# Optimization experiments

Hardware: AMD Instinct MI355X
Metric: run time of the kernel (lower is better)

The kernel has to match this reference:

```python
import jax, jax.numpy as jnp
import numpy as np

FEATURES = 256
HIDDEN = 256
NUM_BINS = 10
NUM_BLOCKS = 2
MULT = 2 * NUM_BINS + 1  # tails=None -> widths(K) + heights(K+1)
MIN_BW = 1e-3
MIN_BH = 1e-3
BATCH = 8192


def _build_masks():
    # nflows MADE sequential degrees
    in_deg = np.arange(1, FEATURES + 1)
    hid_deg = np.arange(HIDDEN) % max(1, FEATURES - 1) + min(1, FEATURES - 1)
    m0 = (hid_deg[:, None] >= in_deg[None, :]).astype(np.float32)   # [H, F]
    mh = (hid_deg[:, None] >= hid_deg[None, :]).astype(np.float32)  # [H, H]
    out_deg = np.repeat(in_deg, MULT)                               # feature-major tiling (nflows _tile)
    mf = (out_deg[:, None] > hid_deg[None, :]).astype(np.float32)   # [F*MULT, H]
    return jnp.asarray(m0), jnp.asarray(mh), jnp.asarray(mf)

MASK0, MASKH, MASKF = _build_masks()


def setup_inputs() -> dict:
    key = jax.random.key(0)
    ks = jax.random.split(key, 7)
    s = 1.0 / np.sqrt(HIDDEN)
    return {
        "inputs": jax.random.uniform(ks[0], (BATCH, FEATURES), dtype=jnp.float32),
        "W0": jax.random.normal(ks[1], (HIDDEN, FEATURES), dtype=jnp.float32) * s,
        "b0": jax.random.normal(ks[2], (HIDDEN,), dtype=jnp.float32) * 0.01,
        "Wb": jax.random.normal(ks[3], (2 * NUM_BLOCKS, HIDDEN, HIDDEN), dtype=jnp.float32) * s,
        "bb": jax.random.normal(ks[4], (2 * NUM_BLOCKS, HIDDEN), dtype=jnp.float32) * 0.01,
        "Wf": jax.random.normal(ks[5], (FEATURES * MULT, HIDDEN), dtype=jnp.float32) * s,
        "bf": jax.random.normal(ks[6], (FEATURES * MULT,), dtype=jnp.float32) * 0.01,
    }


def _made(x, W0, b0, Wb, bb, Wf, bf):
    h = x @ (W0 * MASK0).T + b0
    for i in range(NUM_BLOCKS):  # pre-activation masked residual blocks
        t = jax.nn.relu(h)
        t = t @ (Wb[2 * i] * MASKH).T + bb[2 * i]
        t = jax.nn.relu(t)
        t = t @ (Wb[2 * i + 1] * MASKH).T + bb[2 * i + 1]
        h = h + t
    return h @ (Wf * MASKF).T + bf  # [B, F*MULT]


def _quadratic_spline(x, uw, uh):
    # x: [B,F]; uw: [B,F,K]; uh: [B,F,K+1]
    widths = jax.nn.softmax(uw, axis=-1)
    widths = MIN_BW + (1.0 - MIN_BW * NUM_BINS) * widths
    hexp = jnp.exp(uh)
    area = jnp.sum(0.5 * (hexp[..., :-1] + hexp[..., 1:]) * widths, axis=-1, keepdims=True)
    heights = hexp / area
    heights = MIN_BH + (1.0 - MIN_BH) * heights

    cdf = jnp.cumsum(0.5 * (heights[..., :-1] + heights[..., 1:]) * widths, axis=-1)
    cdf = cdf.at[..., -1].set(1.0)
    cdf = jnp.pad(cdf, [(0, 0), (0, 0), (1, 0)])
    locs = jnp.cumsum(widths, axis=-1)
    locs = locs.at[..., -1].set(1.0)
    locs = jnp.pad(locs, [(0, 0), (0, 0), (1, 0)])

    # searchsorted: sum(x >= knots) - 1, clamped into valid bins
    idx = jnp.clip(jnp.sum(x[..., None] >= locs, axis=-1) - 1, 0, NUM_BINS - 1)
    g = lambda t, i: jnp.take_along_axis(t, i[..., None], axis=-1)[..., 0]

    loc = g(locs, idx)
    w = g(widths, idx)
    lcdf = g(cdf, idx)
    hl = g(heights, idx)
    hr = g(heights, idx + 1)

    a = 0.5 * (hr - hl) * w
    b = hl * w
    alpha = (x - loc) / w
    out = jnp.clip(a * alpha * alpha + b * alpha + lcdf, 0.0, 1.0)
    logabsdet = jnp.log(alpha * (hr - hl) + hl)
    return out, jnp.sum(logabsdet, axis=-1)  # sum_except_batch


def reference(inputs, W0, b0, Wb, bb, Wf, bf):
    params = _made(inputs, W0, b0, Wb, bb, Wf, bf)
    tp = params.reshape(inputs.shape[0], FEATURES, MULT)
    scale = 1.0 / np.sqrt(HIDDEN).astype(np.float32)
    uw = tp[..., :NUM_BINS] * scale
    uh = tp[..., NUM_BINS:] * scale
    return _quadratic_spline(inputs, uw, uh)
```

## Files before the change

kernel.cpp:

```cpp
#include <hip/hip_runtime.h>

typedef _Float16 f16;
typedef f16 f16x8 __attribute__((ext_vector_type(8)));
typedef float f32x4 __attribute__((ext_vector_type(4)));

#define MFMA(A,B,C) __builtin_amdgcn_mfma_f32_16x16x32_f16(A,B,C,0,0,0)

#define PTRUNK 0u
#define PHEAD  655360u

__device__ __forceinline__ void fsplit(float v, f16& hi, f16& lo) {
    hi = (f16)v;
    lo = (f16)(v - (float)hi);
}

__global__ __launch_bounds__(256) void prep_kernel(
    const float* __restrict__ W0, const float* __restrict__ Wb,
    const float* __restrict__ Wf, unsigned char* __restrict__ wsb)
{
    __shared__ f16 sm[16][264];
    const int b = blockIdx.x, t = threadIdx.x;
    const int cr = t >> 4, kc = t & 15;

    if (b < 80) {
        const int mat = b >> 4, ct = b & 15;
        const int c = ct * 16 + cr;
        const int cd = c % 255;
        const float* src = ((mat == 0) ? W0 : (Wb + (mat - 1) * 65536)) + c * 256;
        #pragma unroll
        for (int u = 0; u < 4; ++u) {
            const int k = kc * 16 + u * 4;
            float4 v = *(const float4*)(src + k);
            float vv[4] = {v.x, v.y, v.z, v.w};
            #pragma unroll
            for (int e = 0; e < 4; ++e) {
                int kk = k + e;
                int kd = (mat == 0) ? kk : (kk % 255);
                sm[cr][kk] = (cd >= kd) ? (f16)vv[e] : (f16)0.f;
            }
        }
        __syncthreads();
        const int ks = t >> 5, ln = t & 31;
        #pragma unroll
        for (int rep = 0; rep < 2; ++rep) {
            const int L = ln + rep * 32;
            const int li = L & 15, lg = L >> 4;
            f16x8 v = *(const f16x8*)&sm[li][ks * 32 + lg * 8];
            ((f16x8*)(wsb + PTRUNK))[(mat * 128 + ks * 16 + ct) * 64 + L] = v;
        }
    } else {
        const int hb = b - 80;
        const int bly = hb / 21, ct = hb - bly * 21;
        const int cl = ct * 16 + cr;
        const int fw = cl / 21;
        const int f  = bly * 16 + fw;
        const int m  = cl - fw * 21;
        const float* src = Wf + (f * 21 + m) * 256;
        #pragma unroll
        for (int u = 0; u < 4; ++u) {
            const int k = kc * 16 + u * 4;
            float4 v = *(const float4*)(src + k);
            float vv[4] = {v.x, v.y, v.z, v.w};
            #pragma unroll
            for (int e = 0; e < 4; ++e) {
                int kk = k + e;
                int jd = kk % 255;
                sm[cr][(kk + 1) & 255] = (f > jd) ? (f16)vv[e] : (f16)0.f;
            }
        }
        __syncthreads();
        const int ks = t >> 5, ln = t & 31;
        #pragma unroll
        for (int rep = 0; rep < 2; ++rep) {
            const int L = ln + rep * 32;
            const int li = L & 15, lg = L >> 4;
            f16x8 v = *(const f16x8*)&sm[li][ks * 32 + lg * 8];
            ((f16x8*)(wsb + PHEAD))[((bly * 8 + ks) * 21 + ct) * 64 + L] = v;
        }
    }
}

__global__ __launch_bounds__(256, 2) void mega_kernel(
    const float* __restrict__ x, const unsigned char* __restrict__ wsb,
    const float* __restrict__ b0, const float* __restrict__ bb,
    const float* __restrict__ bfp, float* __restrict__ out,
    float* __restrict__ lad)
{
    __shared__ f16  Ah[2][16][280];
    __shared__ f16  Al[2][16][280];
    __shared__ float prm[4][16][100];
    __shared__ float ladp[4][16];

    const int t = threadIdx.x, lane = t & 63;
    const int wu = __builtin_amdgcn_readfirstlane(t >> 6);
    const int li = lane & 15, lg = lane >> 4;
    const int r0 = blockIdx.x * 16;

    {
        int row = t >> 4, cb = (t & 15) * 16;
        const float* xr = x + (r0 + row) * 256 + cb;
        f16 hi[16], lo[16];
        #pragma unroll
        for (int j = 0; j < 16; j += 4) {
            float4 v4 = *(const float4*)(xr + j);
            fsplit(v4.x, hi[j],     lo[j]);
            fsplit(v4.y, hi[j + 1], lo[j + 1]);
            fsplit(v4.z, hi[j + 2], lo[j + 2]);
            fsplit(v4.w, hi[j + 3], lo[j + 3]);
        }
        *(f16x8*)&Ah[0][row][cb]     = *(f16x8*)&hi[0];
        *(f16x8*)&Ah[0][row][cb + 8] = *(f16x8*)&hi[8];
        *(f16x8*)&Al[0][row][cb]     = *(f16x8*)&lo[0];
        *(f16x8*)&Al[0][row][cb + 8] = *(f16x8*)&lo[8];
    }
    __syncthreads();

    const f16x8* wt = (const f16x8*)(wsb + PTRUNK);
    const f16x8* wh = (const f16x8*)(wsb + PHEAD);

    f32x4 h[4], acc[4];
    const int nkp = 2 * wu + 2;

    auto gemm = [&](int mat, int src, int add7, const float* __restrict__ bias) {
        #pragma unroll
        for (int ci = 0; ci < 4; ++ci) acc[ci] = (f32x4){0.f, 0.f, 0.f, 0.f};
        const int tot = nkp + add7;
        const f16x8* wb = wt + mat * 8192;
        f16x8 bA[4], bB[4];
        #pragma unroll
        for (int ci = 0; ci < 4; ++ci) bA[ci] = wb[(wu * 4 + ci) * 64 + lane];
        for (int s = 0; s < tot; s += 2) {
            const int ks1 = (s + 1 < nkp) ? (s + 1) : 7;
            #pragma unroll
            for (int ci = 0; ci < 4; ++ci)
                bB[ci] = wb[(ks1 * 16 + wu * 4 + ci) * 64 + lane];
            {
                const int ks = (s < nkp) ? s : 7;
                f16x8 ah = *(const f16x8*)&Ah[src][li][ks * 32 + lg * 8];
                f16x8 al = *(const f16x8*)&Al[src][li][ks * 32 + lg * 8];
                #pragma unroll
                for (int ci = 0; ci < 4; ++ci) {
                    acc[ci] = MFMA(al, bA[ci], acc[ci]);
                    acc[ci] = MFMA(ah, bA[ci], acc[ci]);
                }
            }
            const int ks2 = (s + 2 < nkp) ? (s + 2) : 7;
            #pragma unroll
            for (int ci = 0; ci < 4; ++ci)
                bA[ci] = wb[(ks2 * 16 + wu * 4 + ci) * 64 + lane];
            if (s + 1 < tot) {
                f16x8 ah = *(const f16x8*)&Ah[src][li][ks1 * 32 + lg * 8];
                f16x8 al = *(const f16x8*)&Al[src][li][ks1 * 32 + lg * 8];
                #pragma unroll
                for (int ci = 0; ci < 4; ++ci) {
                    acc[ci] = MFMA(al, bB[ci], acc[ci]);
                    acc[ci] = MFMA(ah, bB[ci], acc[ci]);
                }
            }
        }
        #pragma unroll
        for (int ci = 0; ci < 4; ++ci) {
            float bv = bias[(wu * 4 + ci) * 16 + li];
            #pragma unroll
            for (int q = 0; q < 4; ++q) acc[ci][q] += bv;
        }
    };

    auto store_act = [&](int dst, f32x4* s, bool relu, bool rot) {
        #pragma unroll
        for (int ci = 0; ci < 4; ++ci) {
            int c  = (wu * 4 + ci) * 16 + li;
            int cc = rot ? ((c + 1) & 255) : c;
            #pragma unroll
            for (int q = 0; q < 4; ++q) {
                float v = s[ci][q];
                if (relu) v = fmaxf(v, 0.f);
                f16 hi, lo; fsplit(v, hi, lo);
                Ah[dst][lg * 4 + q][cc] = hi;
                Al[dst][lg * 4 + q][cc] = lo;
            }
        }
    };

    gemm(0, 0, 0, b0);
    #pragma unroll
    for (int ci = 0; ci < 4; ++ci) h[ci] = acc[ci];
    store_act(1, acc, true, false);
    __syncthreads();

    gemm(1, 1, (wu < 3) ? 1 : 0, bb + 0);
    store_act(0, acc, true, false);
    __syncthreads();

    gemm(2, 0, (wu < 3) ? 1 : 0, bb + 256);
    #pragma unroll
    for (int ci = 0; ci < 4; ++ci) h[ci] += acc[ci];
    store_act(1, h, true, false);
    __syncthreads();

    gemm(3, 1, (wu < 3) ? 1 : 0, bb + 512);
    store_act(0, acc, true, false);
    __syncthreads();

    gemm(4, 0, (wu < 3) ? 1 : 0, bb + 768);
    #pragma unroll
    for (int ci = 0; ci < 4; ++ci) h[ci] += acc[ci];
    store_act(1, h, false, true);
    __syncthreads();

    float ladreg = 0.f;

    for (int ib = 0; ib < 4; ++ib) {
        const int bly = ib * 4 + wu;
        const int nl = (bly + 2) >> 1;
        const int f0 = bly * 16;

        #pragma unroll
        for (int pass = 0; pass < 4; ++pass) {
            const int f = f0 + pass * 4 + lg;
            const float xv = x[(r0 + li) * 256 + f];

            f32x4 hacc[6];
            #pragma unroll
            for (int ci = 0; ci < 6; ++ci) hacc[ci] = (f32x4){0.f, 0.f, 0.f, 0.f};

            f16x8 bA[6], bB[6];
            #pragma unroll
            for (int ci = 0; ci < 6; ++ci)
                bA[ci] = wh[((bly * 8) * 21 + pass * 5 + ci) * 64 + lane];

            for (int s = 0; s < nl; s += 2) {
                const int s1 = (s + 1 < nl) ? (s + 1) : (nl - 1);
                #pragma unroll
                for (int ci = 0; ci < 6; ++ci)
                    bB[ci] = wh[((bly * 8 + s1) * 21 + pass * 5 + ci) * 64 + lane];
                {
                    f16x8 ah = *(const f16x8*)&Ah[1][li][s * 32 + lg * 8];
                    f16x8 al = *(const f16x8*)&Al[1][li][s * 32 + lg * 8];
                    #pragma unroll
                    for (int ci = 0; ci < 6; ++ci) {
                        hacc[ci] = MFMA(al, bA[ci], hacc[ci]);
                        hacc[ci] = MFMA(ah, bA[ci], hacc[ci]);
                    }
                }
                const int s2 = (s + 2 < nl) ? (s + 2) : (nl - 1);
                #pragma unroll
                for (int ci = 0; ci < 6; ++ci)
                    bA[ci] = wh[((bly * 8 + s2) * 21 + pass * 5 + ci) * 64 + lane];
                if (s + 1 < nl) {
                    f16x8 ah = *(const f16x8*)&Ah[1][li][s1 * 32 + lg * 8];
                    f16x8 al = *(const f16x8*)&Al[1][li][s1 * 32 + lg * 8];
                    #pragma unroll
                    for (int ci = 0; ci < 6; ++ci) {
                        hacc[ci] = MFMA(al, bB[ci], hacc[ci]);
                        hacc[ci] = MFMA(ah, bB[ci], hacc[ci]);
                    }
                }
            }

            #pragma unroll
            for (int ci = 0; ci < 6; ++ci) {
                int cl = (pass * 5 + ci) * 16 + li;
                int fw = cl / 21;
                int m  = cl - fw * 21;
                if (fw >= pass * 4 && fw < pass * 4 + 4) {
                    float bv = bfp[f0 * 21 + cl];
                    #pragma unroll
                    for (int q = 0; q < 4; ++q)
                        prm[wu][lg * 4 + q][(fw - pass * 4) * 24 + m] =
                            (hacc[ci][q] + bv) * 0.0625f;
                }
            }

            float p[21];
            #pragma unroll
            for (int m = 0; m < 21; ++m) p[m] = prm[wu][li][lg * 24 + m];

            float wmax = p[0];
            #pragma unroll
            for (int i = 1; i < 10; ++i) wmax = fmaxf(wmax, p[i]);
            float ew[10]; float wsum = 0.f;
            #pragma unroll
            for (int i = 0; i < 10; ++i) { ew[i] = __expf(p[i] - wmax); wsum += ew[i]; }
            float winv = 1.0f / wsum;
            float wid[10];
            #pragma unroll
            for (int i = 0; i < 10; ++i) wid[i] = 1.0e-3f + 0.99f * ew[i] * winv;

            float hx[11];
            #pragma unroll
            for (int i = 0; i < 11; ++i) hx[i] = __expf(p[10 + i]);
            float area = 0.f;
            #pragma unroll
            for (int i = 0; i < 10; ++i) area += 0.5f * (hx[i] + hx[i + 1]) * wid[i];
            float ainv = 1.0f / area;
            float hts[11];
            #pragma unroll
            for (int i = 0; i < 11; ++i) hts[i] = 1.0e-3f + 0.999f * hx[i] * ainv;

            float cdf[11], locs[11];
            cdf[0] = 0.f; locs[0] = 0.f;
            float ca = 0.f, la = 0.f;
            #pragma unroll
            for (int i = 0; i < 10; ++i) {
                ca += 0.5f * (hts[i] + hts[i + 1]) * wid[i];
                la += wid[i];
                cdf[i + 1] = ca; locs[i + 1] = la;
            }
            cdf[10] = 1.0f; locs[10] = 1.0f;

            int cntk = 0;
            #pragma unroll
            for (int i = 0; i < 11; ++i) cntk += (xv >= locs[i]) ? 1 : 0;
            int idx = cntk - 1;
            idx = idx < 0 ? 0 : (idx > 9 ? 9 : idx);

            float loc = 0.f, ww = 0.f, lc = 0.f, hl = 0.f, hr = 0.f;
            #pragma unroll
            for (int i = 0; i < 10; ++i)
                if (i == idx) { loc = locs[i]; ww = wid[i]; lc = cdf[i]; hl = hts[i]; hr = hts[i + 1]; }

            float aq  = 0.5f * (hr - hl) * ww;
            float bq2 = hl * ww;
            float al2 = (xv - loc) / ww;
            float y = (aq * al2 + bq2) * al2 + lc;
            y = fminf(fmaxf(y, 0.f), 1.f);
            out[(r0 + li) * 256 + f] = y;

            ladreg += __logf(al2 * (hr - hl) + hl);
        }
    }

    ladreg += __shfl_xor(ladreg, 16);
    ladreg += __shfl_xor(ladreg, 32);
    if (lane < 16) ladp[wu][lane] = ladreg;
    __syncthreads();
    if (t < 16)
        lad[r0 + t] = ladp[0][t] + ladp[1][t] + ladp[2][t] + ladp[3][t];
}

extern "C" void kernel_launch(void* const* d_in, const int* in_sizes, int n_in,
                              void* d_out, int out_size, void* d_ws, size_t ws_size,
                              hipStream_t stream)
{
    const float* x  = (const float*)d_in[0];
    const float* W0 = (const float*)d_in[1];
    const float* b0 = (const float*)d_in[2];
    const float* Wb = (const float*)d_in[3];
    const float* bb = (const float*)d_in[4];
    const float* Wf = (const float*)d_in[5];
    const float* bf = (const float*)d_in[6];

    float* out = (float*)d_out;
    float* lad = out + 8192 * 256;
    unsigned char* wsb = (unsigned char*)d_ws;

    prep_kernel<<<416, 256, 0, stream>>>(W0, Wb, Wf, wsb);
    mega_kernel<<<512, 256, 0, stream>>>(x, wsb, b0, bb, bf, out, lad);
}
```

Measured before the change: 149.6 us.

## Double rows per block to 32 with 8 waves and balanced triangular column pairing

```diff
diff --git a/kernel.cpp b/kernel.cpp
--- a/kernel.cpp
+++ b/kernel.cpp
@@ -8,6 +8,8 @@
 
 #define PTRUNK 0u
 #define PHEAD  655360u
+
+#define SMEM_BYTES 80384
 
 __device__ __forceinline__ void fsplit(float v, f16& hi, f16& lo) {
     hi = (f16)v;
@@ -80,24 +82,27 @@
     }
 }
 
-__global__ __launch_bounds__(256, 2) void mega_kernel(
+__global__ __launch_bounds__(512, 2) void mega_kernel(
     const float* __restrict__ x, const unsigned char* __restrict__ wsb,
     const float* __restrict__ b0, const float* __restrict__ bb,
     const float* __restrict__ bfp, float* __restrict__ out,
     float* __restrict__ lad)
 {
-    __shared__ f16  Ah[2][16][280];
-    __shared__ f16  Al[2][16][280];
-    __shared__ float prm[4][16][100];
-    __shared__ float ladp[4][16];
+    extern __shared__ unsigned char smem[];
+    f16 (*Ah1)[264] = (f16(*)[264])(smem);
+    f16 (*Al1)[264] = (f16(*)[264])(smem + 16896);
+    f16 (*Ah0)[264] = (f16(*)[264])(smem + 33792);
+    f16 (*Al0)[264] = (f16(*)[264])(smem + 50688);
+    float* prm      = (float*)(smem + 33792);
+    float* ladp     = (float*)(smem + 79360);
 
     const int t = threadIdx.x, lane = t & 63;
     const int wu = __builtin_amdgcn_readfirstlane(t >> 6);
     const int li = lane & 15, lg = lane >> 4;
-    const int r0 = blockIdx.x * 16;
+    const int r0 = blockIdx.x * 32;
 
     {
-        int row = t >> 4, cb = (t & 15) * 16;
+        const int row = t >> 4, cb = (t & 15) * 16;
         const float* xr = x + (r0 + row) * 256 + cb;
         f16 hi[16], lo[16];
         #pragma unroll
@@ -108,235 +113,276 @@
             fsplit(v4.z, hi[j + 2], lo[j + 2]);
             fsplit(v4.w, hi[j + 3], lo[j + 3]);
         }
-        *(f16x8*)&Ah[0][row][cb]     = *(f16x8*)&hi[0];
-        *(f16x8*)&Ah[0][row][cb + 8] = *(f16x8*)&hi[8];
-        *(f16x8*)&Al[0][row][cb]     = *(f16x8*)&lo[0];
-        *(f16x8*)&Al[0][row][cb + 8] = *(f16x8*)&lo[8];
+        *(f16x8*)&Ah0[row][cb]     = *(f16x8*)&hi[0];
+        *(f16x8*)&Ah0[row][cb + 8] = *(f16x8*)&hi[8];
+        *(f16x8*)&Al0[row][cb]     = *(f16x8*)&lo[0];
+        *(f16x8*)&Al0[row][cb + 8] = *(f16x8*)&lo[8];
     }
     __syncthreads();
 
     const f16x8* wt = (const f16x8*)(wsb + PTRUNK);
     const f16x8* wh = (const f16x8*)(wsb + PHEAD);
 
-    f32x4 h[4], acc[4];
-    const int nkp = 2 * wu + 2;
-
-    auto gemm = [&](int mat, int src, int add7, const float* __restrict__ bias) {
-        #pragma unroll
-        for (int ci = 0; ci < 4; ++ci) acc[ci] = (f32x4){0.f, 0.f, 0.f, 0.f};
-        const int tot = nkp + add7;
+    const int ctA = wu, ctB = 15 - wu;
+    const int nkA = (ctA >> 1) + 1;
+    const int nkB = (ctB >> 1) + 1;
+
+    f32x4 acc[2][2], h[2][2];
+
+    auto gemm = [&](int mat, f16 (*Sh)[264], f16 (*Sl)[264],
+                    const float* __restrict__ bias) {
+        const int a7 = (mat > 0) ? 1 : 0;
+        const int tB = nkB + ((a7 && nkB < 8) ? 1 : 0);
         const f16x8* wb = wt + mat * 8192;
-        f16x8 bA[4], bB[4];
-        #pragma unroll
-        for (int ci = 0; ci < 4; ++ci) bA[ci] = wb[(wu * 4 + ci) * 64 + lane];
-        for (int s = 0; s < tot; s += 2) {
-            const int ks1 = (s + 1 < nkp) ? (s + 1) : 7;
-            #pragma unroll
-            for (int ci = 0; ci < 4; ++ci)
-                bB[ci] = wb[(ks1 * 16 + wu * 4 + ci) * 64 + lane];
-            {
-                const int ks = (s < nkp) ? s : 7;
-                f16x8 ah = *(const f16x8*)&Ah[src][li][ks * 32 + lg * 8];
-                f16x8 al = *(const f16x8*)&Al[src][li][ks * 32 + lg * 8];
+        f16x8 bfA[9], bfB[9];
+        #pragma unroll
+        for (int s = 0; s < 9; ++s) {
+            if (s < tB) {
+                const int ks = (s < nkB) ? s : 7;
+                bfB[s] = wb[(ks * 16 + ctB) * 64 + lane];
+                if (ks < nkA || (a7 && ks == 7))
+                    bfA[s] = wb[(ks * 16 + ctA) * 64 + lane];
+            }
+        }
+        #pragma unroll
+        for (int ci = 0; ci < 2; ++ci)
+            #pragma unroll
+            for (int rt = 0; rt < 2; ++rt)
+                acc[ci][rt] = (f32x4){0.f, 0.f, 0.f, 0.f};
+        #pragma unroll
+        for (int s = 0; s < 9; ++s) {
+            if (s < tB) {
+                const int ks = (s < nkB) ? s : 7;
+                const int ko = ks * 32 + lg * 8;
+                f16x8 ah0 = *(const f16x8*)&Sh[li][ko];
+                f16x8 al0 = *(const f16x8*)&Sl[li][ko];
+                f16x8 ah1 = *(const f16x8*)&Sh[16 + li][ko];
+                f16x8 al1 = *(const f16x8*)&Sl[16 + li][ko];
+                acc[1][0] = MFMA(al0, bfB[s], acc[1][0]);
+                acc[1][0] = MFMA(ah0, bfB[s], acc[1][0]);
+                acc[1][1] = MFMA(al1, bfB[s], acc[1][1]);
+                acc[1][1] = MFMA(ah1, bfB[s], acc[1][1]);
+                if (ks < nkA || (a7 && ks == 7)) {
+                    acc[0][0] = MFMA(al0, bfA[s], acc[0][0]);
+                    acc[0][0] = MFMA(ah0, bfA[s], acc[0][0]);
+                    acc[0][1] = MFMA(al1, bfA[s], acc[0][1]);
+                    acc[0][1] = MFMA(ah1, bfA[s], acc[0][1]);
+                }
+            }
+        }
+        const float bvA = bias[ctA * 16 + li];
+        const float bvB = bias[ctB * 16 + li];
+        #pragma unroll
+        for (int rt = 0; rt < 2; ++rt)
+            #pragma unroll
+            for (int q = 0; q < 4; ++q) {
+                acc[0][rt][q] += bvA;
+                acc[1][rt][q] += bvB;
+            }
+    };
+
+    auto store_act = [&](f16 (*Dh)[264], f16 (*Dl)[264], f32x4 (&s)[2][2],
+                         bool relu, bool rot) {
+        #pragma unroll
+        for (int ci = 0; ci < 2; ++ci) {
+            const int c  = (ci ? ctB : ctA) * 16 + li;
+            const int cc = rot ? ((c + 1) & 255) : c;
+            #pragma unroll
+            for (int rt = 0; rt < 2; ++rt)
                 #pragma unroll
-                for (int ci = 0; ci < 4; ++ci) {
-                    acc[ci] = MFMA(al, bA[ci], acc[ci]);
-                    acc[ci] = MFMA(ah, bA[ci], acc[ci]);
+                for (int q = 0; q < 4; ++q) {
+                    float v = s[ci][rt][q];
+                    if (relu) v = fmaxf(v, 0.f);
+                    f16 hi, lo; fsplit(v, hi, lo);
+                    Dh[rt * 16 + lg * 4 + q][cc] = hi;
+                    Dl[rt * 16 + lg * 4 + q][cc] = lo;
                 }
-            }
-            const int ks2 = (s + 2 < nkp) ? (s + 2) : 7;
-            #pragma unroll
-            for (int ci = 0; ci < 4; ++ci)
-                bA[ci] = wb[(ks2 * 16 + wu * 4 + ci) * 64 + lane];
-            if (s + 1 < tot) {
-                f16x8 ah = *(const f16x8*)&Ah[src][li][ks1 * 32 + lg * 8];
-                f16x8 al = *(const f16x8*)&Al[src][li][ks1 * 32 + lg * 8];
+        }
+    };
+
+    gemm(0, Ah0, Al0, b0);
+    #pragma unroll
+    for (int ci = 0; ci < 2; ++ci)
+        #pragma unroll
+        for (int rt = 0; rt < 2; ++rt) h[ci][rt] = acc[ci][rt];
+    store_act(Ah1, Al1, acc, true, false);
+    __syncthreads();
+
+    gemm(1, Ah1, Al1, bb);
+    store_act(Ah0, Al0, acc, true, false);
+    __syncthreads();
+
+    gemm(2, Ah0, Al0, bb + 256);
+    #pragma unroll
+    for (int ci = 0; ci < 2; ++ci)
+        #pragma unroll
+        for (int rt = 0; rt < 2; ++rt) h[ci][rt] += acc[ci][rt];
+    store_act(Ah1, Al1, h, true, false);
+    __syncthreads();
+
+    gemm(3, Ah1, Al1, bb + 512);
+    store_act(Ah0, Al0, acc, true, false);
+    __syncthreads();
+
+    gemm(4, Ah0, Al0, bb + 768);
+    #pragma unroll
+    for (int ci = 0; ci < 2; ++ci)
+        #pragma unroll
+        for (int rt = 0; rt < 2; ++rt) h[ci][rt] += acc[ci][rt];
+    store_act(Ah1, Al1, h, false, true);
+    __syncthreads();
+
+    float lr0 = 0.f, lr1 = 0.f;
+
+    auto do_half = [&](const f32x4* hacc, int hp, float xv, int pass, int f0,
+                       int fme, float& lr) {
+        #pragma unroll
+        for (int ci = 0; ci < 6; ++ci) {
+            const int cl = (pass * 5 + ci) * 16 + li;
+            const int fw = cl / 21;
+            const int m  = cl - fw * 21;
+            if (fw >= pass * 4 && fw < pass * 4 + 4) {
+                const float bv = bfp[f0 * 21 + cl];
                 #pragma unroll
-                for (int ci = 0; ci < 4; ++ci) {
-                    acc[ci] = MFMA(al, bB[ci], acc[ci]);
-                    acc[ci] = MFMA(ah, bB[ci], acc[ci]);
-                }
-            }
-        }
-        #pragma unroll
-        for (int ci = 0; ci < 4; ++ci) {
-            float bv = bias[(wu * 4 + ci) * 16 + li];
-            #pragma unroll
-            for (int q = 0; q < 4; ++q) acc[ci][q] += bv;
-        }
+                for (int q = 0; q < 4; ++q)
+                    prm[(wu * 16 + lg * 4 + q) * 89 + (fw - pass * 4) * 22 + m] =
+                        (hacc[ci][q] + bv) * 0.0625f;
+            }
+        }
+        float p[21];
+        #pragma unroll
+        for (int m = 0; m < 21; ++m)
+            p[m] = prm[(wu * 16 + li) * 89 + lg * 22 + m];
+
+        float wmax = p[0];
+        #pragma unroll
+        for (int i = 1; i < 10; ++i) wmax = fmaxf(wmax, p[i]);
+        float ew[10]; float wsum = 0.f;
+        #pragma unroll
+        for (int i = 0; i < 10; ++i) { ew[i] = __expf(p[i] - wmax); wsum += ew[i]; }
+        const float winv = 1.0f / wsum;
+        float wid[10];
+        #pragma unroll
+        for (int i = 0; i < 10; ++i) wid[i] = 1.0e-3f + 0.99f * ew[i] * winv;
+
+        float hx[11];
+        #pragma unroll
+        for (int i = 0; i < 11; ++i) hx[i] = __expf(p[10 + i]);
+        float area = 0.f;
+        #pragma unroll
+        for (int i = 0; i < 10; ++i) area += (hx[i] + hx[i + 1]) * wid[i];
+        const float ainv = 2.0f / area;
+        float hts[11];
+        #pragma unroll
+        for (int i = 0; i < 11; ++i) hts[i] = 1.0e-3f + 0.999f * hx[i] * ainv;
+
+        float la = wid[0];
+        float ca = 0.5f * (hts[0] + hts[1]) * wid[0];
+        float loc = 0.f, ww = wid[0], lc = 0.f, hl = hts[0], hr = hts[1];
+        #pragma unroll
+        for (int i = 1; i < 10; ++i) {
+            const bool sel = (xv >= la);
+            loc = sel ? la : loc;
+            ww  = sel ? wid[i] : ww;
+            lc  = sel ? ca : lc;
+            hl  = sel ? hts[i] : hl;
+            hr  = sel ? hts[i + 1] : hr;
+            la += wid[i];
+            ca += 0.5f * (hts[i] + hts[i + 1]) * wid[i];
+        }
+        const float al2 = (xv - loc) / ww;
+        const float dh  = hr - hl;
+        float y = (0.5f * dh * ww * al2 + hl * ww) * al2 + lc;
+        y = fminf(fmaxf(y, 0.f), 1.f);
+        out[(r0 + hp * 16 + li) * 256 + fme] = y;
+        lr += __logf(al2 * dh + hl);
     };
 
-    auto store_act = [&](int dst, f32x4* s, bool relu, bool rot) {
-        #pragma unroll
-        for (int ci = 0; ci < 4; ++ci) {
-            int c  = (wu * 4 + ci) * 16 + li;
-            int cc = rot ? ((c + 1) & 255) : c;
-            #pragma unroll
-            for (int q = 0; q < 4; ++q) {
-                float v = s[ci][q];
-                if (relu) v = fmaxf(v, 0.f);
-                f16 hi, lo; fsplit(v, hi, lo);
-                Ah[dst][lg * 4 + q][cc] = hi;
-                Al[dst][lg * 4 + q][cc] = lo;
-            }
-        }
-    };
-
-    gemm(0, 0, 0, b0);
     #pragma unroll
-    for (int ci = 0; ci < 4; ++ci) h[ci] = acc[ci];
-    store_act(1, acc, true, false);
-    __syncthreads();
-
-    gemm(1, 1, (wu < 3) ? 1 : 0, bb + 0);
-    store_act(0, acc, true, false);
-    __syncthreads();
-
-    gemm(2, 0, (wu < 3) ? 1 : 0, bb + 256);
-    #pragma unroll
-    for (int ci = 0; ci < 4; ++ci) h[ci] += acc[ci];
-    store_act(1, h, true, false);
-    __syncthreads();
-
-    gemm(3, 1, (wu < 3) ? 1 : 0, bb + 512);
-    store_act(0, acc, true, false);
-    __syncthreads();
-
-    gemm(4, 0, (wu < 3) ? 1 : 0, bb + 768);
-    #pragma unroll
-    for (int ci = 0; ci < 4; ++ci) h[ci] += acc[ci];
-    store_act(1, h, false, true);
-    __syncthreads();
-
-    float ladreg = 0.f;
-
-    for (int ib = 0; ib < 4; ++ib) {
-        const int bly = ib * 4 + wu;
-        const int nl = (bly + 2) >> 1;
-        const int f0 = bly * 16;
+    for (int ib = 0; ib < 2; ++ib) {
+        const int bly = ib ? (15 - wu) : wu;
+        const int nl  = (bly + 2) >> 1;
+        const int f0  = bly * 16;
+        const int bly8 = bly * 8;
 
         #pragma unroll
         for (int pass = 0; pass < 4; ++pass) {
-            const int f = f0 + pass * 4 + lg;
-            const float xv = x[(r0 + li) * 256 + f];
-
-            f32x4 hacc[6];
-            #pragma unroll
-            for (int ci = 0; ci < 6; ++ci) hacc[ci] = (f32x4){0.f, 0.f, 0.f, 0.f};
-
-            f16x8 bA[6], bB[6];
+            const int p5  = pass * 5;
+            const int fme = f0 + pass * 4 + lg;
+            const float xv0 = x[(r0 + li) * 256 + fme];
+            const float xv1 = x[(r0 + 16 + li) * 256 + fme];
+
+            f32x4 pA[6], pB[6];
+            #pragma unroll
+            for (int ci = 0; ci < 6; ++ci) {
+                pA[ci] = (f32x4){0.f, 0.f, 0.f, 0.f};
+                pB[ci] = (f32x4){0.f, 0.f, 0.f, 0.f};
+            }
+
+            f16x8 c0[6], c1[6];
             #pragma unroll
             for (int ci = 0; ci < 6; ++ci)
-                bA[ci] = wh[((bly * 8) * 21 + pass * 5 + ci) * 64 + lane];
-
+                c0[ci] = wh[(bly8 * 21 + p5 + ci) * 64 + lane];
+
+            __builtin_amdgcn_s_setprio(1);
             for (int s = 0; s < nl; s += 2) {
-                const int s1 = (s + 1 < nl) ? (s + 1) : (nl - 1);
+                const int s1 = (s + 1 < nl) ? s + 1 : 0;
                 #pragma unroll
                 for (int ci = 0; ci < 6; ++ci)
-                    bB[ci] = wh[((bly * 8 + s1) * 21 + pass * 5 + ci) * 64 + lane];
+                    c1[ci] = wh[((bly8 + s1) * 21 + p5 + ci) * 64 + lane];
                 {
-                    f16x8 ah = *(const f16x8*)&Ah[1][li][s * 32 + lg * 8];
-                    f16x8 al = *(const f16x8*)&Al[1][li][s * 32 + lg * 8];
+                    const int ko = s * 32 + lg * 8;
+                    f16x8 ah0 = *(const f16x8*)&Ah1[li][ko];
+                    f16x8 al0 = *(const f16x8*)&Al1[li][ko];
+                    f16x8 ah1 = *(const f16x8*)&Ah1[16 + li][ko];
+                    f16x8 al1 = *(const f16x8*)&Al1[16 + li][ko];
                     #pragma unroll
                     for (int ci = 0; ci < 6; ++ci) {
-                        hacc[ci] = MFMA(al, bA[ci], hacc[ci]);
-                        hacc[ci] = MFMA(ah, bA[ci], hacc[ci]);
+                        pA[ci] = MFMA(al0, c0[ci], pA[ci]);
+                        pA[ci] = MFMA(ah0, c0[ci], pA[ci]);
+                        pB[ci] = MFMA(al1, c0[ci], pB[ci]);
+                        pB[ci] = MFMA(ah1, c0[ci], pB[ci]);
                     }
                 }
-                const int s2 = (s + 2 < nl) ? (s + 2) : (nl - 1);
+                const int s2 = (s + 2 < nl) ? s + 2 : 0;
                 #pragma unroll
                 for (int ci = 0; ci < 6; ++ci)
-                    bA[ci] = wh[((bly * 8 + s2) * 21 + pass * 5 + ci) * 64 + lane];
+                    c0[ci] = wh[((bly8 + s2) * 21 + p5 + ci) * 64 + lane];
                 if (s + 1 < nl) {
-                    f16x8 ah = *(const f16x8*)&Ah[1][li][s1 * 32 + lg * 8];
-                    f16x8 al = *(const f16x8*)&Al[1][li][s1 * 32 + lg * 8];
+                    const int ko = s1 * 32 + lg * 8;
+                    f16x8 ah0 = *(const f16x8*)&Ah1[li][ko];
+                    f16x8 al0 = *(const f16x8*)&Al1[li][ko];
+                    f16x8 ah1 = *(const f16x8*)&Ah1[16 + li][ko];
+                    f16x8 al1 = *(const f16x8*)&Al1[16 + li][ko];
                     #pragma unroll
                     for (int ci = 0; ci < 6; ++ci) {
-                        hacc[ci] = MFMA(al, bB[ci], hacc[ci]);
-                        hacc[ci] = MFMA(ah, bB[ci], hacc[ci]);
+                        pA[ci] = MFMA(al0, c1[ci], pA[ci]);
+                        pA[ci] = MFMA(ah0, c1[ci], pA[ci]);
+                        pB[ci] = MFMA(al1, c1[ci], pB[ci]);
+                        pB[ci] = MFMA(ah1, c1[ci], pB[ci]);
                     }
                 }
             }
-
-            #pragma unroll
-            for (int ci = 0; ci < 6; ++ci) {
-                int cl = (pass * 5 + ci) * 16 + li;
-                int fw = cl / 21;
-                int m  = cl - fw * 21;
-                if (fw >= pass * 4 && fw < pass * 4 + 4) {
-                    float bv = bfp[f0 * 21 + cl];
-                    #pragma unroll
-                    for (int q = 0; q < 4; ++q)
-                        prm[wu][lg * 4 + q][(fw - pass * 4) * 24 + m] =
-                            (hacc[ci][q] + bv) * 0.0625f;
-                }
-            }
-
-            float p[21];
-            #pragma unroll
-            for (int m = 0; m < 21; ++m) p[m] = prm[wu][li][lg * 24 + m];
-
-            float wmax = p[0];
-            #pragma unroll
-            for (int i = 1; i < 10; ++i) wmax = fmaxf(wmax, p[i]);
-            float ew[10]; float wsum = 0.f;
-            #pragma unroll
-            for (int i = 0; i < 10; ++i) { ew[i] = __expf(p[i] - wmax); wsum += ew[i]; }
-            float winv = 1.0f / wsum;
-            float wid[10];
-            #pragma unroll
-            for (int i = 0; i < 10; ++i) wid[i] = 1.0e-3f + 0.99f * ew[i] * winv;
-
-            float hx[11];
-            #pragma unroll
-            for (int i = 0; i < 11; ++i) hx[i] = __expf(p[10 + i]);
-            float area = 0.f;
-            #pragma unroll
-            for (int i = 0; i < 10; ++i) area += 0.5f * (hx[i] + hx[i + 1]) * wid[i];
-            float ainv = 1.0f / area;
-            float hts[11];
-            #pragma unroll
-            for (int i = 0; i < 11; ++i) hts[i] = 1.0e-3f + 0.999f * hx[i] * ainv;
-
-            float cdf[11], locs[11];
-            cdf[0] = 0.f; locs[0] = 0.f;
-            float ca = 0.f, la = 0.f;
-            #pragma unroll
-            for (int i = 0; i < 10; ++i) {
-                ca += 0.5f * (hts[i] + hts[i + 1]) * wid[i];
-                la += wid[i];
-                cdf[i + 1] = ca; locs[i + 1] = la;
-            }
-            cdf[10] = 1.0f; locs[10] = 1.0f;
-
-            int cntk = 0;
-            #pragma unroll
-            for (int i = 0; i < 11; ++i) cntk += (xv >= locs[i]) ? 1 : 0;
-            int idx = cntk - 1;
-            idx = idx < 0 ? 0 : (idx > 9 ? 9 : idx);
-
-            float loc = 0.f, ww = 0.f, lc = 0.f, hl = 0.f, hr = 0.f;
-            #pragma unroll
-            for (int i = 0; i < 10; ++i)
-                if (i == idx) { loc = locs[i]; ww = wid[i]; lc = cdf[i]; hl = hts[i]; hr = hts[i + 1]; }
-
-            float aq  = 0.5f * (hr - hl) * ww;
-            float bq2 = hl * ww;
-            float al2 = (xv - loc) / ww;
-            float y = (aq * al2 + bq2) * al2 + lc;
-            y = fminf(fmaxf(y, 0.f), 1.f);
-            out[(r0 + li) * 256 + f] = y;
-
-            ladreg += __logf(al2 * (hr - hl) + hl);
+            __builtin_amdgcn_s_setprio(0);
+
+            do_half(pA, 0, xv0, pass, f0, fme, lr0);
+            do_half(pB, 1, xv1, pass, f0, fme, lr1);
         }
     }
 
-    ladreg += __shfl_xor(ladreg, 16);
-    ladreg += __shfl_xor(ladreg, 32);
-    if (lane < 16) ladp[wu][lane] = ladreg;
-    __syncthreads();
-    if (t < 16)
-        lad[r0 + t] = ladp[0][t] + ladp[1][t] + ladp[2][t] + ladp[3][t];
+    lr0 += __shfl_xor(lr0, 16); lr0 += __shfl_xor(lr0, 32);
+    lr1 += __shfl_xor(lr1, 16); lr1 += __shfl_xor(lr1, 32);
+    if (lane < 16) {
+        ladp[wu * 32 + lane]      = lr0;
+        ladp[wu * 32 + 16 + lane] = lr1;
+    }
+    __syncthreads();
+    if (t < 32) {
+        float s = 0.f;
+        #pragma unroll
+        for (int w2 = 0; w2 < 8; ++w2) s += ladp[w2 * 32 + t];
+        lad[r0 + t] = s;
+    }
 }
 
 extern "C" void kernel_launch(void* const* d_in, const int* in_sizes, int n_in,
@@ -355,6 +401,9 @@
     float* lad = out + 8192 * 256;
     unsigned char* wsb = (unsigned char*)d_ws;
 
+    hipFuncSetAttribute(reinterpret_cast<const void*>(mega_kernel),
+                        hipFuncAttributeMaxDynamicSharedMemorySize, SMEM_BYTES);
+
     prep_kernel<<<416, 256, 0, stream>>>(W0, Wb, Wf, wsb);
-    mega_kernel<<<512, 256, 0, stream>>>(x, wsb, b0, bb, bf, out, lad);
+    mega_kernel<<<256, 512, SMEM_BYTES, stream>>>(x, wsb, b0, bb, bf, out, lad);
 }
```

After: 136.9 us. -8.5%, faster.
